# Kernel optimization log

Hardware: AMD Instinct MI355X
Metric: run time of the kernel (lower is better)

Reference implementation:

```python
import jax, jax.numpy as jnp
import numpy as np

N_GRID = 128
DX = 1.0 / N_GRID
INV_DX = float(N_GRID)
DT = 1e-4
P_VOL = (DX * 0.5) ** 2
P_RHO = 1.0
P_MASS = P_VOL * P_RHO
E_MOD, NU = 1000.0, 0.2
MU_0 = E_MOD / (2.0 * (1.0 + NU))
LAMBDA_0 = E_MOD * NU / ((1.0 + NU) * (1.0 - 2.0 * NU))
N_PART = 1_000_000


def setup_inputs() -> dict:
    key = jax.random.key(0)
    k1, k2, k3, k4, k5 = jax.random.split(key, 5)
    # particles strictly inside the domain so the 3x3 stencil stays in-grid
    x = 0.1 + 0.8 * jax.random.uniform(k1, (N_PART, 2), jnp.float32)
    v = 0.5 * jax.random.normal(k2, (N_PART, 2), jnp.float32)
    C = 0.1 * jax.random.normal(k3, (N_PART, 2, 2), jnp.float32)
    F = jnp.eye(2, dtype=jnp.float32)[None] + 0.01 * jax.random.normal(k4, (N_PART, 2, 2), jnp.float32)
    material = jax.random.randint(k5, (N_PART,), 0, 3, jnp.int32)
    Jp = jnp.ones((N_PART,), jnp.float32)
    return {"x": x, "v": v, "C": C, "F": F, "material": material, "Jp": Jp}


def mpm_step(x, v, C, F, material, Jp):
    # --- particle kinematics / constitutive model ---
    base = jnp.floor(x * INV_DX - 0.5).astype(jnp.int32)          # (N,2)
    fx = x * INV_DX - base.astype(x.dtype)                        # (N,2)
    w = jnp.stack([0.5 * (1.5 - fx) ** 2,
                   0.75 - (fx - 1.0) ** 2,
                   0.5 * (fx - 0.5) ** 2], axis=0)                # (3,N,2)

    F = F + DT * jnp.einsum('nij,njk->nik', C, F)
    m0 = material == 0
    m2 = material == 2
    h = jnp.where(material == 1, 0.3, jnp.exp(10.0 * (1.0 - Jp)))
    mu = jnp.where(m0, 0.0, MU_0 * h)
    lam = LAMBDA_0 * h

    U, sig, Vh = jnp.linalg.svd(F)                                # batched 2x2 SVD
    clamped = jnp.clip(sig, 1.0 - 2.5e-2, 1.0 + 4.5e-3)
    Jp = jnp.where(m2, Jp * jnp.prod(sig / clamped, axis=-1), Jp)
    sig = jnp.where(m2[:, None], clamped, sig)
    J = jnp.prod(sig, axis=-1)

    eye = jnp.eye(2, dtype=F.dtype)
    F_liquid = eye[None] * jnp.sqrt(J)[:, None, None]             # J**(1/n_dim), n_dim=2
    F_snow = jnp.einsum('nij,nj,njk->nik', U, sig, Vh)
    F = jnp.where(m0[:, None, None], F_liquid,
                  jnp.where(m2[:, None, None], F_snow, F))

    R = jnp.einsum('nij,njk->nik', U, Vh)
    stress = (2.0 * mu[:, None, None] * jnp.einsum('nij,nkj->nik', F - R, F)
              + eye[None] * (lam * J * (J - 1.0))[:, None, None])
    stress = (-DT * P_VOL * 4.0 * INV_DX ** 2) * stress
    affine = stress + P_MASS * C                                  # (N,2,2)

    mom = P_MASS * v - jnp.einsum('nij,nj->ni', affine, x)        # (N,2)

    # --- P2G scatter over 3x3 stencil ---
    grid_v = jnp.zeros((N_GRID * N_GRID, 2), x.dtype)
    grid_m = jnp.zeros((N_GRID * N_GRID,), x.dtype)
    grid_aff = jnp.zeros((N_GRID * N_GRID, 2, 2), x.dtype)
    for i in range(3):
        for j in range(3):
            weight = w[i, :, 0] * w[j, :, 1]                      # (N,)
            idx = (base[:, 0] + i) * N_GRID + (base[:, 1] + j)
            grid_v = grid_v.at[idx].add(weight[:, None] * mom)
            grid_aff = grid_aff.at[idx].add(weight[:, None, None] * affine)
            grid_m = grid_m.at[idx].add(weight * P_MASS)
    grid_v = grid_v.reshape(N_GRID, N_GRID, 2)
    grid_m = grid_m.reshape(N_GRID, N_GRID)
    grid_aff = grid_aff.reshape(N_GRID, N_GRID, 2, 2)

    gi = jnp.arange(N_GRID, dtype=x.dtype)
    grid_x = jnp.stack(jnp.meshgrid(gi, gi, indexing='ij'), axis=-1) * DX   # (G,G,2)
    grid_v = grid_v + jnp.einsum('abij,abj->abi', grid_aff, grid_x)

    # --- grid normalization, gravity, boundary clamps ---
    nonempty = grid_m > 0
    safe_m = jnp.where(nonempty, grid_m, 1.0)
    grid_v = jnp.where(nonempty[..., None], grid_v / safe_m[..., None], grid_v)
    grid_v = grid_v.at[:, :, 1].add(jnp.where(nonempty, -DT * 50.0, 0.0))

    row = jnp.arange(N_GRID)
    vx, vy = grid_v[..., 0], grid_v[..., 1]
    vx = jnp.where(row[:, None] < 3, jnp.maximum(vx, 0.0), vx)
    vx = jnp.where(row[:, None] >= N_GRID - 2, jnp.minimum(vx, 0.0), vx)
    vy = jnp.where(row[None, :] < 3, jnp.maximum(vy, 0.0), vy)
    vy = jnp.where(row[None, :] >= N_GRID - 2, jnp.minimum(vy, 0.0), vy)
    grid_v = jnp.stack([vx, vy], axis=-1)

    # --- G2P gather over 3x3 stencil ---
    new_v = jnp.zeros_like(v)
    new_C = jnp.zeros_like(C)
    for i in range(3):
        for j in range(3):
            weight = w[i, :, 0] * w[j, :, 1]
            g_v = grid_v[base[:, 0] + i, base[:, 1] + j]          # (N,2)
            node = (base + jnp.array([i, j], base.dtype)).astype(x.dtype) * DX
            new_v = new_v + weight[:, None] * g_v
            new_C = new_C + weight[:, None, None] * g_v[:, :, None] * node[:, None, :]
    new_C = (new_C - new_v[:, :, None] * x[:, None, :]) * (4.0 * INV_DX ** 2)

    x_new = x + DT * new_v
    return x_new, new_v, new_C, F, material, Jp


def reference(x, v, C, F, material, Jp):
    return mpm_step(x, v, C, F, material, Jp)
```

## Files before the change

kernel.cpp:

```cpp
#include <hip/hip_runtime.h>

#define NPART 1000000
#define NGRID 128
#define NNODES (NGRID * NGRID)
#define NBINS 64
#define BINCAP 26624
#define SUBW 18
#define SUBN (SUBW * SUBW)
#define P2G_SUB 8
#define P2G_THREADS 512
#define PS_CHUNK 4
#define PS_BLOCKS 977
#define PS_PART (256 * PS_CHUNK)

#define FPSCALE 281474976710656.0f
#define FPINV   3.552713678800501e-15
#define WSCALE  16777216.0f
#define WINV    5.9604644775390625e-8

#define OUT_X   0
#define OUT_V   2000000
#define OUT_C   4000000
#define OUT_F   8000000
#define OUT_MAT 12000000
#define OUT_JP  13000000

__device__ __forceinline__ void quad_weights(float fx, float w[3]) {
    w[0] = 0.5f * (1.5f - fx) * (1.5f - fx);
    w[1] = 0.75f - (fx - 1.0f) * (fx - 1.0f);
    w[2] = 0.5f * (fx - 0.5f) * (fx - 0.5f);
}

struct PhysOut {
    float o00, o01, o10, o11;
    float aff00, aff01, aff10, aff11;
    float mom0, mom1;
    float jp_new;
};

__device__ __forceinline__ PhysOut particle_phys(
    float2 xx, float2 vv, float4 Cm, float4 Fin, int mat, float jp)
{
    const float DT = 1e-4f;
    const float P_MASS = 1.52587890625e-05f;
    const float MU_0 = (float)(1000.0 / (2.0 * 1.2));
    const float LAMBDA_0 = (float)(200.0 / 0.72);
    const float SCALE = -1e-4f;

    float F00 = Fin.x + DT * (Cm.x * Fin.x + Cm.y * Fin.z);
    float F01 = Fin.y + DT * (Cm.x * Fin.y + Cm.y * Fin.w);
    float F10 = Fin.z + DT * (Cm.z * Fin.x + Cm.w * Fin.z);
    float F11 = Fin.w + DT * (Cm.z * Fin.y + Cm.w * Fin.w);

    float h = (mat == 1) ? 0.3f : expf(10.0f * (1.0f - jp));
    float mu = (mat == 0) ? 0.0f : MU_0 * h;
    float lam = LAMBDA_0 * h;

    float Es = 0.5f * (F00 + F11), Fs = 0.5f * (F00 - F11);
    float Gs = 0.5f * (F01 + F10), Hs = 0.5f * (F10 - F01);
    float q2 = Es * Es + Hs * Hs;
    float r2 = Fs * Fs + Gs * Gs;
    float Qs = sqrtf(q2);
    float Rs = sqrtf(r2);
    float s1 = Qs + Rs, s2 = Qs - Rs;
    float cdif = 1.0f, sdif = 0.0f;
    if (q2 > 1e-30f) { float rq = 1.0f / Qs; cdif = Es * rq; sdif = Hs * rq; }
    float csum = 1.0f, ssum = 0.0f;
    if (r2 > 1e-30f) { float rr = 1.0f / Rs; csum = Fs * rr; ssum = Gs * rr; }
    float cucv = 0.5f * (cdif + csum);
    float susv = 0.5f * (cdif - csum);
    float cusv = 0.5f * (ssum - sdif);
    float sucv = 0.5f * (ssum + sdif);

    float c1 = fminf(fmaxf(s1, 1.0f - 2.5e-2f), 1.0f + 4.5e-3f);
    float c2 = fminf(fmaxf(s2, 1.0f - 2.5e-2f), 1.0f + 4.5e-3f);
    float jp_new = jp;
    float sg1 = s1, sg2 = s2;
    if (mat == 2) {
        jp_new = jp * (s1 / c1) * (s2 / c2);
        sg1 = c1;
        sg2 = c2;
    }
    float J = sg1 * sg2;

    float R00 = cdif, R01 = -sdif;
    float R10 = sdif, R11 = cdif;

    float o00, o01, o10, o11;
    if (mat == 0) {
        float sq = sqrtf(J);
        o00 = sq; o01 = 0.0f; o10 = 0.0f; o11 = sq;
    } else if (mat == 2) {
        o00 = sg1 * cucv + sg2 * susv;
        o01 = sg1 * cusv - sg2 * sucv;
        o10 = sg1 * sucv - sg2 * cusv;
        o11 = sg1 * susv + sg2 * cucv;
    } else {
        o00 = F00; o01 = F01; o10 = F10; o11 = F11;
    }

    float A00 = o00 - R00, A01 = o01 - R01, A10 = o10 - R10, A11 = o11 - R11;
    float S00 = A00 * o00 + A01 * o01;
    float S01 = A00 * o10 + A01 * o11;
    float S10 = A10 * o00 + A11 * o01;
    float S11 = A10 * o10 + A11 * o11;
    float ljj = lam * J * (J - 1.0f);

    PhysOut po;
    po.o00 = o00; po.o01 = o01; po.o10 = o10; po.o11 = o11;
    po.aff00 = SCALE * (2.0f * mu * S00 + ljj) + P_MASS * Cm.x;
    po.aff01 = SCALE * (2.0f * mu * S01)       + P_MASS * Cm.y;
    po.aff10 = SCALE * (2.0f * mu * S10)       + P_MASS * Cm.z;
    po.aff11 = SCALE * (2.0f * mu * S11 + ljj) + P_MASS * Cm.w;
    po.mom0 = P_MASS * vv.x - (po.aff00 * xx.x + po.aff01 * xx.y);
    po.mom1 = P_MASS * vv.y - (po.aff10 * xx.x + po.aff11 * xx.y);
    po.jp_new = jp_new;
    return po;
}

__device__ __forceinline__ int tile_of(float2 xx) {
    int b0 = (int)floorf(xx.x * 128.0f - 0.5f);
    int b1 = (int)floorf(xx.y * 128.0f - 0.5f);
    return ((b0 >> 4) << 3) | (b1 >> 4);
}

__global__ __launch_bounds__(256) void phys_scatter_kernel(
    const float2* __restrict__ x, const float2* __restrict__ v,
    const float4* __restrict__ C, const float4* __restrict__ F,
    const int* __restrict__ material, const float* __restrict__ Jp,
    int* __restrict__ binCursor, float* __restrict__ out, float4* __restrict__ rec)
{
    __shared__ int lh[NBINS];
    __shared__ int lpre[NBINS];
    __shared__ int lbase[NBINS];
    __shared__ int s_total;
    __shared__ float4 srec0[PS_PART];
    __shared__ float4 srec1[PS_PART];
    __shared__ int spos[PS_PART];

    int tid = threadIdx.x;
    if (tid < NBINS) lh[tid] = 0;
    __syncthreads();
    int base = blockIdx.x * PS_PART;

    float2 xs[PS_CHUNK], vs[PS_CHUNK];
    float4 Cs[PS_CHUNK], Fs[PS_CHUNK];
    float jps[PS_CHUNK];
    int ms[PS_CHUNK], pk[PS_CHUNK];

    #pragma unroll
    for (int c = 0; c < PS_CHUNK; ++c) {
        int n = base + c * 256 + tid;
        if (n < NPART) {
            xs[c] = x[n]; vs[c] = v[n]; Cs[c] = C[n]; Fs[c] = F[n];
            ms[c] = material[n]; jps[c] = Jp[n];
            int t = tile_of(xs[c]);
            int r = atomicAdd(&lh[t], 1);
            pk[c] = (t << 16) | r;
        } else pk[c] = -1;
    }
    __syncthreads();
    if (tid < NBINS) {
        int c = lh[tid];
        int inc = c;
        #pragma unroll
        for (int d = 1; d < 64; d <<= 1) {
            int y = __shfl_up(inc, d);
            if (tid >= d) inc += y;
        }
        lpre[tid] = inc - c;
        if (tid == NBINS - 1) s_total = inc;
        lbase[tid] = tid * BINCAP + (c ? atomicAdd(&binCursor[tid], c) : 0);
    }
    __syncthreads();

    #pragma unroll
    for (int c = 0; c < PS_CHUNK; ++c) {
        if (pk[c] < 0) continue;
        int n = base + c * 256 + tid;
        PhysOut po = particle_phys(xs[c], vs[c], Cs[c], Fs[c], ms[c], jps[c]);
        ((float4*)(out + OUT_F))[n] = make_float4(po.o00, po.o01, po.o10, po.o11);
        out[OUT_MAT + n] = (float)ms[c];
        out[OUT_JP + n] = po.jp_new;
        int t = pk[c] >> 16, r = pk[c] & 0xffff;
        int loc = lpre[t] + r;
        srec0[loc] = make_float4(xs[c].x, xs[c].y, po.mom0, po.mom1);
        srec1[loc] = make_float4(po.aff00, po.aff01, po.aff10, po.aff11);
        spos[loc] = lbase[t] + r;
    }
    __syncthreads();

    int total = s_total;
    for (int k = tid; k < total; k += 256) {
        int pos = spos[k];
        rec[2 * pos]     = srec0[k];
        rec[2 * pos + 1] = srec1[k];
    }
}

__global__ __launch_bounds__(P2G_THREADS) void p2g_kernel(
    const float4* __restrict__ rec, const int* __restrict__ binCursor,
    float* __restrict__ part)
{
    __shared__ unsigned long long s_v0[SUBN], s_v1[SUBN];
    __shared__ unsigned int s_m[SUBN];
    int tid = threadIdx.x;
    int tile = blockIdx.x >> 3;
    int sub  = blockIdx.x & (P2G_SUB - 1);
    for (int i = tid; i < SUBN; i += P2G_THREADS) {
        s_v0[i] = 0ull; s_v1[i] = 0ull; s_m[i] = 0u;
    }
    __syncthreads();
    int start = tile * BINCAP;
    int cnt = binCursor[tile];
    int t0 = (tile >> 3) << 4;
    int t1 = (tile & 7) << 4;
    const float DX = 1.0f / 128.0f;

    for (int p = sub * P2G_THREADS + tid; p < cnt; p += P2G_SUB * P2G_THREADS) {
        float4 r0 = rec[2 * (start + p)];
        float4 r1 = rec[2 * (start + p) + 1];
        float xg0 = r0.x * 128.0f, xg1 = r0.y * 128.0f;
        int b0 = (int)floorf(xg0 - 0.5f), b1 = (int)floorf(xg1 - 0.5f);
        float fx0 = xg0 - (float)b0, fx1 = xg1 - (float)b1;
        float wx[3], wy[3];
        quad_weights(fx0, wx);
        quad_weights(fx1, wy);
        int l0 = b0 - t0, l1 = b1 - t1;
        #pragma unroll
        for (int i = 0; i < 3; ++i) {
            float nx0 = (float)(b0 + i) * DX;
            #pragma unroll
            for (int j = 0; j < 3; ++j) {
                float wt = wx[i] * wy[j];
                float nx1 = (float)(b1 + j) * DX;
                int l = (l0 + i) * SUBW + (l1 + j);
                long long q0 = (long long)(wt * (r0.z + r1.x * nx0 + r1.y * nx1) * FPSCALE);
                long long q1 = (long long)(wt * (r0.w + r1.z * nx0 + r1.w * nx1) * FPSCALE);
                unsigned int qm = (unsigned int)(wt * WSCALE);
                atomicAdd(&s_v0[l], (unsigned long long)q0);
                atomicAdd(&s_v1[l], (unsigned long long)q1);
                atomicAdd(&s_m[l], qm);
            }
        }
    }
    __syncthreads();
    float* slab = part + (size_t)blockIdx.x * (3 * SUBN);
    for (int l = tid; l < SUBN; l += P2G_THREADS) {
        slab[l]            = (float)((double)(long long)s_v0[l] * FPINV);
        slab[SUBN + l]     = (float)((double)(long long)s_v1[l] * FPINV);
        slab[2 * SUBN + l] = (float)((double)s_m[l] * WINV);
    }
}

__global__ __launch_bounds__(256) void grid_kernel(
    const float* __restrict__ part, float2* __restrict__ gvn)
{
    int t = blockIdx.x * 256 + threadIdx.x;
    int idx = t >> 3;
    int sub = t & 7;
    if (idx >= NNODES) return;
    const float P_MASS = 1.52587890625e-05f;
    int gi = idx >> 7, gj = idx & 127;
    int li = gi & 15, lj = gj & 15, ti = gi >> 4, tj = gj >> 4;

    int tis[2], l0s[2]; int ni = 1; tis[0] = ti; l0s[0] = li;
    if (li < 2 && ti > 0) { tis[1] = ti - 1; l0s[1] = li + 16; ni = 2; }
    int tjs[2], l1s[2]; int nj = 1; tjs[0] = tj; l1s[0] = lj;
    if (lj < 2 && tj > 0) { tjs[1] = tj - 1; l1s[1] = lj + 16; nj = 2; }

    float s0 = 0.f, s1 = 0.f, sw = 0.f;
    for (int a = 0; a < ni; ++a) {
        for (int b = 0; b < nj; ++b) {
            int tile2 = tis[a] * 8 + tjs[b];
            int l = l0s[a] * SUBW + l1s[b];
            const float* sb = part + (size_t)(tile2 * P2G_SUB + sub) * (3 * SUBN) + l;
            s0 += sb[0];
            s1 += sb[SUBN];
            sw += sb[2 * SUBN];
        }
    }
    #pragma unroll
    for (int m = 4; m >= 1; m >>= 1) {
        s0 += __shfl_xor(s0, m);
        s1 += __shfl_xor(s1, m);
        sw += __shfl_xor(sw, m);
    }
    if (sub == 0) {
        float m = sw * P_MASS;
        if (m > 0.f) {
            float rm = 1.0f / m;
            s0 *= rm;
            s1 *= rm;
            s1 -= 5e-3f;
        }
        if (gi < 3) s0 = fmaxf(s0, 0.0f);
        if (gi >= NGRID - 2) s0 = fminf(s0, 0.0f);
        if (gj < 3) s1 = fmaxf(s1, 0.0f);
        if (gj >= NGRID - 2) s1 = fminf(s1, 0.0f);
        gvn[idx] = make_float2(s0, s1);
    }
}

__global__ __launch_bounds__(256) void g2p_kernel(
    const float2* __restrict__ x, const float2* __restrict__ gvn,
    float* __restrict__ out)
{
    int n = blockIdx.x * blockDim.x + threadIdx.x;
    if (n >= NPART) return;
    const float DX = 1.0f / 128.0f;
    const float DT = 1e-4f;
    const float K4 = 65536.0f;

    float2 xx = x[n];
    float xg0 = xx.x * 128.0f, xg1 = xx.y * 128.0f;
    int b0 = (int)floorf(xg0 - 0.5f), b1 = (int)floorf(xg1 - 0.5f);
    float fx0 = xg0 - (float)b0, fx1 = xg1 - (float)b1;
    float wx[3], wy[3];
    quad_weights(fx0, wx);
    quad_weights(fx1, wy);

    float nv0 = 0.f, nv1 = 0.f;
    float nC00 = 0.f, nC01 = 0.f, nC10 = 0.f, nC11 = 0.f;
    #pragma unroll
    for (int i = 0; i < 3; ++i) {
        float node0 = (float)(b0 + i) * DX;
        #pragma unroll
        for (int j = 0; j < 3; ++j) {
            float wt = wx[i] * wy[j];
            float2 g = gvn[(b0 + i) * NGRID + (b1 + j)];
            float node1 = (float)(b1 + j) * DX;
            nv0 += wt * g.x;
            nv1 += wt * g.y;
            nC00 += wt * g.x * node0;
            nC01 += wt * g.x * node1;
            nC10 += wt * g.y * node0;
            nC11 += wt * g.y * node1;
        }
    }
    nC00 = (nC00 - nv0 * xx.x) * K4;
    nC01 = (nC01 - nv0 * xx.y) * K4;
    nC10 = (nC10 - nv1 * xx.x) * K4;
    nC11 = (nC11 - nv1 * xx.y) * K4;

    ((float2*)(out + OUT_X))[n] = make_float2(xx.x + DT * nv0, xx.y + DT * nv1);
    ((float2*)(out + OUT_V))[n] = make_float2(nv0, nv1);
    ((float4*)(out + OUT_C))[n] = make_float4(nC00, nC01, nC10, nC11);
}

extern "C" void kernel_launch(void* const* d_in, const int* in_sizes, int n_in,
                              void* d_out, int out_size, void* d_ws, size_t ws_size,
                              hipStream_t stream)
{
    const float2* x = (const float2*)d_in[0];
    const float2* v = (const float2*)d_in[1];
    const float4* C = (const float4*)d_in[2];
    const float4* F = (const float4*)d_in[3];
    const int* material = (const int*)d_in[4];
    const float* Jp = (const float*)d_in[5];
    float* out = (float*)d_out;

    int* binCursor = (int*)d_ws;
    float* part = (float*)((char*)d_ws + 4096);
    float2* gvn = (float2*)((char*)d_ws + (11 << 18));
    float4* rec = (float4*)((char*)d_ws + (4 << 20));

    hipMemsetAsync(binCursor, 0, NBINS * sizeof(int), stream);

    phys_scatter_kernel<<<PS_BLOCKS, 256, 0, stream>>>(x, v, C, F, material, Jp,
                                                       binCursor, out, rec);
    p2g_kernel<<<NBINS * P2G_SUB, P2G_THREADS, 0, stream>>>(rec, binCursor, part);
    grid_kernel<<<(NNODES * 8) / 256, 256, 0, stream>>>(part, gvn);
    g2p_kernel<<<(NPART + 255) / 256, 256, 0, stream>>>(x, gvn, out);
}
```

Baseline: 173.7 us.

## Use float LDS atomics in P2G and cache grid in LDS for G2P

P2G now accumulates momentum and mass with native float shared-memory atomics instead of 64-bit fixed-point integer atomics, removing the quantization and double conversion. G2P becomes a persistent kernel that copies the full 128x128 velocity grid into LDS once per block and gathers stencil values from there instead of global memory. The float atomics make accumulation order-dependent and nondeterministic. The 128 KB LDS footprint limits occupancy to one large block per CU, and each block pays for its own grid copy.

```diff
diff --git a/kernel.cpp b/kernel.cpp
--- a/kernel.cpp
+++ b/kernel.cpp
@@ -12,11 +12,8 @@
 #define PS_CHUNK 4
 #define PS_BLOCKS 977
 #define PS_PART (256 * PS_CHUNK)
-
-#define FPSCALE 281474976710656.0f
-#define FPINV   3.552713678800501e-15
-#define WSCALE  16777216.0f
-#define WINV    5.9604644775390625e-8
+#define G2P_THREADS 1024
+#define G2P_BLOCKS 256
 
 #define OUT_X   0
 #define OUT_V   2000000
@@ -202,13 +199,12 @@
     const float4* __restrict__ rec, const int* __restrict__ binCursor,
     float* __restrict__ part)
 {
-    __shared__ unsigned long long s_v0[SUBN], s_v1[SUBN];
-    __shared__ unsigned int s_m[SUBN];
+    __shared__ float s_v0[SUBN], s_v1[SUBN], s_m[SUBN];
     int tid = threadIdx.x;
     int tile = blockIdx.x >> 3;
     int sub  = blockIdx.x & (P2G_SUB - 1);
     for (int i = tid; i < SUBN; i += P2G_THREADS) {
-        s_v0[i] = 0ull; s_v1[i] = 0ull; s_m[i] = 0u;
+        s_v0[i] = 0.f; s_v1[i] = 0.f; s_m[i] = 0.f;
     }
     __syncthreads();
     int start = tile * BINCAP;
@@ -235,21 +231,18 @@
                 float wt = wx[i] * wy[j];
                 float nx1 = (float)(b1 + j) * DX;
                 int l = (l0 + i) * SUBW + (l1 + j);
-                long long q0 = (long long)(wt * (r0.z + r1.x * nx0 + r1.y * nx1) * FPSCALE);
-                long long q1 = (long long)(wt * (r0.w + r1.z * nx0 + r1.w * nx1) * FPSCALE);
-                unsigned int qm = (unsigned int)(wt * WSCALE);
-                atomicAdd(&s_v0[l], (unsigned long long)q0);
-                atomicAdd(&s_v1[l], (unsigned long long)q1);
-                atomicAdd(&s_m[l], qm);
+                atomicAdd(&s_v0[l], wt * (r0.z + r1.x * nx0 + r1.y * nx1));
+                atomicAdd(&s_v1[l], wt * (r0.w + r1.z * nx0 + r1.w * nx1));
+                atomicAdd(&s_m[l], wt);
             }
         }
     }
     __syncthreads();
     float* slab = part + (size_t)blockIdx.x * (3 * SUBN);
     for (int l = tid; l < SUBN; l += P2G_THREADS) {
-        slab[l]            = (float)((double)(long long)s_v0[l] * FPINV);
-        slab[SUBN + l]     = (float)((double)(long long)s_v1[l] * FPINV);
-        slab[2 * SUBN + l] = (float)((double)s_m[l] * WINV);
+        slab[l]            = s_v0[l];
+        slab[SUBN + l]     = s_v1[l];
+        slab[2 * SUBN + l] = s_m[l];
     }
 }
 
@@ -302,50 +295,60 @@
     }
 }
 
-__global__ __launch_bounds__(256) void g2p_kernel(
+__global__ __launch_bounds__(G2P_THREADS) void g2p_kernel(
     const float2* __restrict__ x, const float2* __restrict__ gvn,
     float* __restrict__ out)
 {
-    int n = blockIdx.x * blockDim.x + threadIdx.x;
-    if (n >= NPART) return;
+    __shared__ float2 s_g[NNODES];
+    int tid = threadIdx.x;
+    {
+        const float4* src = (const float4*)gvn;
+        float4* dst = (float4*)s_g;
+        for (int i = tid; i < NNODES / 2; i += G2P_THREADS) dst[i] = src[i];
+    }
+    __syncthreads();
+
     const float DX = 1.0f / 128.0f;
     const float DT = 1e-4f;
     const float K4 = 65536.0f;
 
-    float2 xx = x[n];
-    float xg0 = xx.x * 128.0f, xg1 = xx.y * 128.0f;
-    int b0 = (int)floorf(xg0 - 0.5f), b1 = (int)floorf(xg1 - 0.5f);
-    float fx0 = xg0 - (float)b0, fx1 = xg1 - (float)b1;
-    float wx[3], wy[3];
-    quad_weights(fx0, wx);
-    quad_weights(fx1, wy);
-
-    float nv0 = 0.f, nv1 = 0.f;
-    float nC00 = 0.f, nC01 = 0.f, nC10 = 0.f, nC11 = 0.f;
-    #pragma unroll
-    for (int i = 0; i < 3; ++i) {
-        float node0 = (float)(b0 + i) * DX;
+    for (int n = blockIdx.x * G2P_THREADS + tid; n < NPART;
+         n += G2P_BLOCKS * G2P_THREADS) {
+        float2 xx = x[n];
+        float xg0 = xx.x * 128.0f, xg1 = xx.y * 128.0f;
+        int b0 = (int)floorf(xg0 - 0.5f), b1 = (int)floorf(xg1 - 0.5f);
+        float fx0 = xg0 - (float)b0, fx1 = xg1 - (float)b1;
+        float wx[3], wy[3];
+        quad_weights(fx0, wx);
+        quad_weights(fx1, wy);
+
+        float nv0 = 0.f, nv1 = 0.f;
+        float nC00 = 0.f, nC01 = 0.f, nC10 = 0.f, nC11 = 0.f;
         #pragma unroll
-        for (int j = 0; j < 3; ++j) {
-            float wt = wx[i] * wy[j];
-            float2 g = gvn[(b0 + i) * NGRID + (b1 + j)];
-            float node1 = (float)(b1 + j) * DX;
-            nv0 += wt * g.x;
-            nv1 += wt * g.y;
-            nC00 += wt * g.x * node0;
-            nC01 += wt * g.x * node1;
-            nC10 += wt * g.y * node0;
-            nC11 += wt * g.y * node1;
-        }
-    }
-    nC00 = (nC00 - nv0 * xx.x) * K4;
-    nC01 = (nC01 - nv0 * xx.y) * K4;
-    nC10 = (nC10 - nv1 * xx.x) * K4;
-    nC11 = (nC11 - nv1 * xx.y) * K4;
-
-    ((float2*)(out + OUT_X))[n] = make_float2(xx.x + DT * nv0, xx.y + DT * nv1);
-    ((float2*)(out + OUT_V))[n] = make_float2(nv0, nv1);
-    ((float4*)(out + OUT_C))[n] = make_float4(nC00, nC01, nC10, nC11);
+        for (int i = 0; i < 3; ++i) {
+            float node0 = (float)(b0 + i) * DX;
+            #pragma unroll
+            for (int j = 0; j < 3; ++j) {
+                float wt = wx[i] * wy[j];
+                float2 g = s_g[(b0 + i) * NGRID + (b1 + j)];
+                float node1 = (float)(b1 + j) * DX;
+                nv0 += wt * g.x;
+                nv1 += wt * g.y;
+                nC00 += wt * g.x * node0;
+                nC01 += wt * g.x * node1;
+                nC10 += wt * g.y * node0;
+                nC11 += wt * g.y * node1;
+            }
+        }
+        nC00 = (nC00 - nv0 * xx.x) * K4;
+        nC01 = (nC01 - nv0 * xx.y) * K4;
+        nC10 = (nC10 - nv1 * xx.x) * K4;
+        nC11 = (nC11 - nv1 * xx.y) * K4;
+
+        ((float2*)(out + OUT_X))[n] = make_float2(xx.x + DT * nv0, xx.y + DT * nv1);
+        ((float2*)(out + OUT_V))[n] = make_float2(nv0, nv1);
+        ((float4*)(out + OUT_C))[n] = make_float4(nC00, nC01, nC10, nC11);
+    }
 }
 
 extern "C" void kernel_launch(void* const* d_in, const int* in_sizes, int n_in,
@@ -371,5 +374,5 @@
                                                        binCursor, out, rec);
     p2g_kernel<<<NBINS * P2G_SUB, P2G_THREADS, 0, stream>>>(rec, binCursor, part);
     grid_kernel<<<(NNODES * 8) / 256, 256, 0, stream>>>(part, gvn);
-    g2p_kernel<<<(NPART + 255) / 256, 256, 0, stream>>>(x, gvn, out);
-}
+    g2p_kernel<<<G2P_BLOCKS, G2P_THREADS, 0, stream>>>(x, gvn, out);
+}
```

New measurement: 359.9 us. 107% more time.

## Fuse grid update into G2P via global fixed-point atomics and shared grid

Applied to the files above, without the earlier changes.

P2G blocks now flush their shared fixed-point sub-grids straight into global 64-bit integer accumulators with atomics, which replaces the per-block partial slabs and the separate grid reduction kernel. The G2P kernel becomes a persistent launch of 256 blocks. Each block rebuilds the whole 128x128 grid velocity field into 128 KB of LDS from the raw sums, then gathers particle stencils from LDS instead of global memory. This removes one kernel launch and the partial-slab traffic. In exchange, every G2P block repeats the 16K-node grid normalization, the memset grows to clear the accumulators, and the large LDS footprint limits occupancy to one block per CU.

```diff
diff --git a/kernel.cpp b/kernel.cpp
--- a/kernel.cpp
+++ b/kernel.cpp
@@ -12,6 +12,8 @@
 #define PS_CHUNK 4
 #define PS_BLOCKS 977
 #define PS_PART (256 * PS_CHUNK)
+#define G2P_THREADS 1024
+#define G2P_BLOCKS 256
 
 #define FPSCALE 281474976710656.0f
 #define FPINV   3.552713678800501e-15
@@ -200,7 +202,9 @@
 
 __global__ __launch_bounds__(P2G_THREADS) void p2g_kernel(
     const float4* __restrict__ rec, const int* __restrict__ binCursor,
-    float* __restrict__ part)
+    unsigned long long* __restrict__ raw_v0,
+    unsigned long long* __restrict__ raw_v1,
+    unsigned long long* __restrict__ raw_m)
 {
     __shared__ unsigned long long s_v0[SUBN], s_v1[SUBN];
     __shared__ unsigned int s_m[SUBN];
@@ -245,48 +249,36 @@
         }
     }
     __syncthreads();
-    float* slab = part + (size_t)blockIdx.x * (3 * SUBN);
     for (int l = tid; l < SUBN; l += P2G_THREADS) {
-        slab[l]            = (float)((double)(long long)s_v0[l] * FPINV);
-        slab[SUBN + l]     = (float)((double)(long long)s_v1[l] * FPINV);
-        slab[2 * SUBN + l] = (float)((double)s_m[l] * WINV);
-    }
-}
-
-__global__ __launch_bounds__(256) void grid_kernel(
-    const float* __restrict__ part, float2* __restrict__ gvn)
-{
-    int t = blockIdx.x * 256 + threadIdx.x;
-    int idx = t >> 3;
-    int sub = t & 7;
-    if (idx >= NNODES) return;
+        unsigned long long a0 = s_v0[l], a1 = s_v1[l];
+        unsigned long long am = (unsigned long long)s_m[l];
+        if (!(a0 | a1 | am)) continue;
+        int li = l / SUBW, lj = l - li * SUBW;
+        int g0 = t0 + li, g1 = t1 + lj;
+        if (g0 >= NGRID || g1 >= NGRID) continue;
+        int g = g0 * NGRID + g1;
+        atomicAdd(&raw_v0[g], a0);
+        atomicAdd(&raw_v1[g], a1);
+        atomicAdd(&raw_m[g], am);
+    }
+}
+
+__global__ __launch_bounds__(G2P_THREADS) void g2p_kernel(
+    const float2* __restrict__ x,
+    const unsigned long long* __restrict__ raw_v0,
+    const unsigned long long* __restrict__ raw_v1,
+    const unsigned long long* __restrict__ raw_m,
+    float* __restrict__ out)
+{
+    __shared__ float2 s_g[NNODES];
+    int tid = threadIdx.x;
     const float P_MASS = 1.52587890625e-05f;
-    int gi = idx >> 7, gj = idx & 127;
-    int li = gi & 15, lj = gj & 15, ti = gi >> 4, tj = gj >> 4;
-
-    int tis[2], l0s[2]; int ni = 1; tis[0] = ti; l0s[0] = li;
-    if (li < 2 && ti > 0) { tis[1] = ti - 1; l0s[1] = li + 16; ni = 2; }
-    int tjs[2], l1s[2]; int nj = 1; tjs[0] = tj; l1s[0] = lj;
-    if (lj < 2 && tj > 0) { tjs[1] = tj - 1; l1s[1] = lj + 16; nj = 2; }
-
-    float s0 = 0.f, s1 = 0.f, sw = 0.f;
-    for (int a = 0; a < ni; ++a) {
-        for (int b = 0; b < nj; ++b) {
-            int tile2 = tis[a] * 8 + tjs[b];
-            int l = l0s[a] * SUBW + l1s[b];
-            const float* sb = part + (size_t)(tile2 * P2G_SUB + sub) * (3 * SUBN) + l;
-            s0 += sb[0];
-            s1 += sb[SUBN];
-            sw += sb[2 * SUBN];
-        }
-    }
-    #pragma unroll
-    for (int m = 4; m >= 1; m >>= 1) {
-        s0 += __shfl_xor(s0, m);
-        s1 += __shfl_xor(s1, m);
-        sw += __shfl_xor(sw, m);
-    }
-    if (sub == 0) {
+
+    for (int idx = tid; idx < NNODES; idx += G2P_THREADS) {
+        float s0 = (float)((double)(long long)raw_v0[idx] * FPINV);
+        float s1 = (float)((double)(long long)raw_v1[idx] * FPINV);
+        float sw = (float)((double)raw_m[idx] * WINV);
+        int gi = idx >> 7, gj = idx & 127;
         float m = sw * P_MASS;
         if (m > 0.f) {
             float rm = 1.0f / m;
@@ -298,54 +290,51 @@
         if (gi >= NGRID - 2) s0 = fminf(s0, 0.0f);
         if (gj < 3) s1 = fmaxf(s1, 0.0f);
         if (gj >= NGRID - 2) s1 = fminf(s1, 0.0f);
-        gvn[idx] = make_float2(s0, s1);
-    }
-}
-
-__global__ __launch_bounds__(256) void g2p_kernel(
-    const float2* __restrict__ x, const float2* __restrict__ gvn,
-    float* __restrict__ out)
-{
-    int n = blockIdx.x * blockDim.x + threadIdx.x;
-    if (n >= NPART) return;
+        s_g[idx] = make_float2(s0, s1);
+    }
+    __syncthreads();
+
     const float DX = 1.0f / 128.0f;
     const float DT = 1e-4f;
     const float K4 = 65536.0f;
 
-    float2 xx = x[n];
-    float xg0 = xx.x * 128.0f, xg1 = xx.y * 128.0f;
-    int b0 = (int)floorf(xg0 - 0.5f), b1 = (int)floorf(xg1 - 0.5f);
-    float fx0 = xg0 - (float)b0, fx1 = xg1 - (float)b1;
-    float wx[3], wy[3];
-    quad_weights(fx0, wx);
-    quad_weights(fx1, wy);
-
-    float nv0 = 0.f, nv1 = 0.f;
-    float nC00 = 0.f, nC01 = 0.f, nC10 = 0.f, nC11 = 0.f;
-    #pragma unroll
-    for (int i = 0; i < 3; ++i) {
-        float node0 = (float)(b0 + i) * DX;
+    for (int n = blockIdx.x * G2P_THREADS + tid; n < NPART;
+         n += G2P_BLOCKS * G2P_THREADS) {
+        float2 xx = x[n];
+        float xg0 = xx.x * 128.0f, xg1 = xx.y * 128.0f;
+        int b0 = (int)floorf(xg0 - 0.5f), b1 = (int)floorf(xg1 - 0.5f);
+        float fx0 = xg0 - (float)b0, fx1 = xg1 - (float)b1;
+        float wx[3], wy[3];
+        quad_weights(fx0, wx);
+        quad_weights(fx1, wy);
+
+        float nv0 = 0.f, nv1 = 0.f;
+        float nC00 = 0.f, nC01 = 0.f, nC10 = 0.f, nC11 = 0.f;
         #pragma unroll
-        for (int j = 0; j < 3; ++j) {
-            float wt = wx[i] * wy[j];
-            float2 g = gvn[(b0 + i) * NGRID + (b1 + j)];
-            float node1 = (float)(b1 + j) * DX;
-            nv0 += wt * g.x;
-            nv1 += wt * g.y;
-            nC00 += wt * g.x * node0;
-            nC01 += wt * g.x * node1;
-            nC10 += wt * g.y * node0;
-            nC11 += wt * g.y * node1;
+        for (int i = 0; i < 3; ++i) {
+            float node0 = (float)(b0 + i) * DX;
+            #pragma unroll
+            for (int j = 0; j < 3; ++j) {
+                float wt = wx[i] * wy[j];
+                float2 g = s_g[(b0 + i) * NGRID + (b1 + j)];
+                float node1 = (float)(b1 + j) * DX;
+                nv0 += wt * g.x;
+                nv1 += wt * g.y;
+                nC00 += wt * g.x * node0;
+                nC01 += wt * g.x * node1;
+                nC10 += wt * g.y * node0;
+                nC11 += wt * g.y * node1;
+            }
         }
-    }
-    nC00 = (nC00 - nv0 * xx.x) * K4;
-    nC01 = (nC01 - nv0 * xx.y) * K4;
-    nC10 = (nC10 - nv1 * xx.x) * K4;
-    nC11 = (nC11 - nv1 * xx.y) * K4;
-
-    ((float2*)(out + OUT_X))[n] = make_float2(xx.x + DT * nv0, xx.y + DT * nv1);
-    ((float2*)(out + OUT_V))[n] = make_float2(nv0, nv1);
-    ((float4*)(out + OUT_C))[n] = make_float4(nC00, nC01, nC10, nC11);
+        nC00 = (nC00 - nv0 * xx.x) * K4;
+        nC01 = (nC01 - nv0 * xx.y) * K4;
+        nC10 = (nC10 - nv1 * xx.x) * K4;
+        nC11 = (nC11 - nv1 * xx.y) * K4;
+
+        ((float2*)(out + OUT_X))[n] = make_float2(xx.x + DT * nv0, xx.y + DT * nv1);
+        ((float2*)(out + OUT_V))[n] = make_float2(nv0, nv1);
+        ((float4*)(out + OUT_C))[n] = make_float4(nC00, nC01, nC10, nC11);
+    }
 }
 
 extern "C" void kernel_launch(void* const* d_in, const int* in_sizes, int n_in,
@@ -361,15 +350,16 @@
     float* out = (float*)d_out;
 
     int* binCursor = (int*)d_ws;
-    float* part = (float*)((char*)d_ws + 4096);
-    float2* gvn = (float2*)((char*)d_ws + (11 << 18));
+    unsigned long long* raw_v0 = (unsigned long long*)((char*)d_ws + 4096);
+    unsigned long long* raw_v1 = raw_v0 + NNODES;
+    unsigned long long* raw_m  = raw_v1 + NNODES;
     float4* rec = (float4*)((char*)d_ws + (4 << 20));
 
-    hipMemsetAsync(binCursor, 0, NBINS * sizeof(int), stream);
+    hipMemsetAsync(d_ws, 0, 4096 + 3 * NNODES * sizeof(unsigned long long), stream);
 
     phys_scatter_kernel<<<PS_BLOCKS, 256, 0, stream>>>(x, v, C, F, material, Jp,
                                                        binCursor, out, rec);
-    p2g_kernel<<<NBINS * P2G_SUB, P2G_THREADS, 0, stream>>>(rec, binCursor, part);
-    grid_kernel<<<(NNODES * 8) / 256, 256, 0, stream>>>(part, gvn);
-    g2p_kernel<<<(NPART + 255) / 256, 256, 0, stream>>>(x, gvn, out);
-}
+    p2g_kernel<<<NBINS * P2G_SUB, P2G_THREADS, 0, stream>>>(rec, binCursor,
+                                                            raw_v0, raw_v1, raw_m);
+    g2p_kernel<<<G2P_BLOCKS, G2P_THREADS, 0, stream>>>(x, raw_v0, raw_v1, raw_m, out);
+}
```

Measured after the change: 166.1 us, median of 2. -4.4%, faster.
